# Kernel tuning notes

Hardware: AMD Instinct MI355X
Metric: run time of the kernel (lower is better)

The kernel has to match this reference:

```python
import jax, jax.numpy as jnp
import numpy as np

D_MODEL, D_STATE, D_CONV, D_INNER, DT_RANK, K = 96, 16, 3, 192, 6, 4
B, H, W = 1, 64, 64


def setup_inputs() -> dict:
    key = jax.random.key(0)
    ks = jax.random.split(key, 10)
    x = jax.random.normal(ks[0], (B, H, W, D_MODEL), jnp.float32)
    in_proj_w = jax.random.normal(ks[1], (2 * D_INNER, D_MODEL), jnp.float32) * 0.02
    conv_w = jax.random.normal(ks[2], (D_INNER, 1, D_CONV, D_CONV), jnp.float32) * 0.1
    conv_b = jnp.zeros((D_INNER,), jnp.float32)
    x_proj_w = jax.random.normal(ks[3], (K, DT_RANK + 2 * D_STATE, D_INNER), jnp.float32) * 0.02
    dt_std = DT_RANK ** -0.5
    dt_w = jax.random.uniform(ks[4], (K, D_INNER, DT_RANK), jnp.float32, -dt_std, dt_std)
    # dt bias init: inv-softplus of dt ~ logUniform(1e-3, 1e-1)
    u = jax.random.uniform(ks[5], (K, D_INNER), jnp.float32)
    dt = jnp.exp(u * (np.log(0.1) - np.log(0.001)) + np.log(0.001)).clip(1e-4)
    dt_b = dt + jnp.log(-jnp.expm1(-dt))
    A_logs = jnp.log(jnp.broadcast_to(jnp.arange(1, D_STATE + 1, dtype=jnp.float32), (K * D_INNER, D_STATE)))
    Ds = jnp.ones((K * D_INNER,), jnp.float32)
    ln_g = jnp.ones((D_INNER,), jnp.float32)
    ln_b = jnp.zeros((D_INNER,), jnp.float32)
    out_proj_w = jax.random.normal(ks[6], (D_MODEL, D_INNER), jnp.float32) * 0.02
    return dict(x=x, in_proj_w=in_proj_w, conv_w=conv_w, conv_b=conv_b, x_proj_w=x_proj_w,
                dt_w=dt_w, dt_b=dt_b, A_logs=A_logs, Ds=Ds, ln_g=ln_g, ln_b=ln_b,
                out_proj_w=out_proj_w)


def _ss2d(x, in_proj_w, conv_w, conv_b, x_proj_w, dt_w, dt_b, A_logs, Ds, ln_g, ln_b, out_proj_w):
    b, h, w, c = x.shape
    L = h * w
    d = conv_w.shape[0]            # d_inner
    n = A_logs.shape[1]            # d_state
    r = dt_w.shape[2]              # dt_rank
    # in_proj + split
    xz = jnp.einsum('bhwc,ec->bhwe', x, in_proj_w)
    xx, z = xz[..., :d], xz[..., d:]
    # depthwise conv (NCHW) + SiLU
    xc = xx.transpose(0, 3, 1, 2)
    pad = (D_CONV - 1) // 2
    xc = jax.lax.conv_general_dilated(xc, conv_w, (1, 1), [(pad, pad), (pad, pad)],
                                      feature_group_count=d) + conv_b[None, :, None, None]
    xc = jax.nn.silu(xc)
    # 4 scan directions: HW, WH, and their reverses
    x_hw = xc.reshape(b, d, L)
    x_wh = xc.transpose(0, 1, 3, 2).reshape(b, d, L)
    xs = jnp.stack([x_hw, x_wh, x_hw[..., ::-1], x_wh[..., ::-1]], axis=1)  # (b,K,d,L)
    x_dbl = jnp.einsum('bkdl,kcd->bkcl', xs, x_proj_w)
    dts, Bs, Cs = x_dbl[:, :, :r], x_dbl[:, :, r:r + n], x_dbl[:, :, r + n:]
    dts = jnp.einsum('bkrl,kdr->bkdl', dts, dt_w)
    delta = jax.nn.softplus(dts + dt_b[None, :, :, None])        # (b,K,d,L)
    A = -jnp.exp(A_logs).reshape(K, d, n)
    # time-major scanned inputs
    dA = jnp.exp(jnp.einsum('bkdl,kdn->lbkdn', delta, A))        # (L,b,K,d,n)
    dBu = jnp.einsum('bkdl,bknl,bkdl->lbkdn', delta, Bs, xs)
    Ct = Cs.transpose(3, 0, 1, 2)                                # (L,b,K,n)
    def step(hst, inp):
        dA_t, dBu_t, C_t = inp
        hst = dA_t * hst + dBu_t
        return hst, jnp.einsum('bkdn,bkn->bkd', hst, C_t)
    h0 = jnp.zeros((b, K, d, n), jnp.float32)
    _, ys = jax.lax.scan(step, h0, (dA, dBu, Ct))                # ys: (L,b,K,d)
    out_y = ys.transpose(1, 2, 3, 0) + xs * Ds.reshape(K, d)[None, :, :, None]
    # recombine directions
    inv = out_y[:, 2:4][..., ::-1]
    y1 = out_y[:, 0]
    y2 = inv[:, 0]
    wh = out_y[:, 1].reshape(b, d, w, h).transpose(0, 1, 3, 2).reshape(b, d, L)
    invwh = inv[:, 1].reshape(b, d, w, h).transpose(0, 1, 3, 2).reshape(b, d, L)
    y = (y1 + y2 + wh + invwh).transpose(0, 2, 1).reshape(b, h, w, d)
    # LayerNorm (eps=1e-5, torch default)
    mu = y.mean(-1, keepdims=True)
    var = ((y - mu) ** 2).mean(-1, keepdims=True)
    y = (y - mu) * jax.lax.rsqrt(var + 1e-5) * ln_g + ln_b
    y = y * jax.nn.silu(z)
    return jnp.einsum('bhwd,cd->bhwc', y, out_proj_w)


def reference(x, in_proj_w, conv_w, conv_b, x_proj_w, dt_w, dt_b, A_logs, Ds, ln_g, ln_b, out_proj_w):
    return _ss2d(x, in_proj_w, conv_w, conv_b, x_proj_w, dt_w, dt_b, A_logs, Ds, ln_g, ln_b, out_proj_w)
```

## Files before the change

### kernel.cpp

```cpp
#include <hip/hip_runtime.h>
#include <hip/hip_bf16.h>

#define LL 4096
#define DM 96
#define DI 192
#define NS 16
#define RK 6
#define RKP 8
#define KD 4
#define CPROJ 38
#define NCH (KD*DI)
#define NC (KD*DI*NS)
#define PT 32
#define WS 196
#define OT 8
#define CHB 7
#define CHN (1<<CHB)
#define CS (LL>>CHB)
#define L2E 1.44269504f

__device__ __forceinline__ float bf2f(unsigned short u){
  unsigned int x = ((unsigned int)u) << 16;
  return __uint_as_float(x);
}
__device__ __forceinline__ float b2f(__hip_bfloat16 v){ return __bfloat162float(v); }

__device__ __forceinline__ void detect_bf16(const unsigned short* __restrict__ xh, int tid, int* sflag){
  if (tid < 64){
    unsigned short u = xh[2*tid];
    int e = (u >> 7) & 0xFF;
    int sane = (e >= 107 && e <= 131) ? 1 : 0;
    unsigned long long m = __ballot(sane);
    if (tid == 0) *sflag = (__popcll(m) >= 32) ? 1 : 0;
  }
}

__device__ __forceinline__ int dir_map(int k, int t){
  if (k==0) return t;
  if (k==1) return ((t&63)<<6) | (t>>6);
  if (k==2) return 4095 - t;
  int u = 4095 - t; return ((u&63)<<6) | (u>>6);
}

struct P12 { const void* p[12]; };

__global__ void __launch_bounds__(384) k_inprojcvt(P12 ptrs, float* __restrict__ cvt,
                         float* __restrict__ xx, float* __restrict__ z) {
  __shared__ float xr[8*DM];
  __shared__ int sflag;
  int tid = threadIdx.x;
  detect_bf16((const unsigned short*)ptrs.p[0], tid, &sflag);
  __syncthreads();
  int f = sflag;
  if (blockIdx.x >= LL/8){
    const int off[12] = {0,36864,38592,38784,67968,72576,73344,85632,86400,86592,86784,105216};
    int i = (blockIdx.x - LL/8)*384 + tid + 36864;
    if (i < 105216){
      int j = 1;
      #pragma unroll
      for (int s = 2; s < 11; s++) if (i >= off[s]) j = s;
      int e = i - off[j];
      const void* src = ptrs.p[j+1];
      cvt[i] = f ? b2f(((const __hip_bfloat16*)src)[e]) : ((const float*)src)[e];
    }
    return;
  }
  int l0 = blockIdx.x * 8;
  if (f){
    const __hip_bfloat16* xb = (const __hip_bfloat16*)ptrs.p[0] + (size_t)l0*DM;
    for (int i = tid; i < 8*DM; i += 384) xr[i] = b2f(xb[i]);
  } else {
    const float* xf = (const float*)ptrs.p[0] + (size_t)l0*DM;
    for (int i = tid; i < 8*DM; i += 384) xr[i] = xf[i];
  }
  __syncthreads();
  int e = tid;
  float acc[8];
  #pragma unroll
  for (int i=0;i<8;i++) acc[i]=0.f;
  const float4* xr4 = (const float4*)xr;
  if (f){
    const ushort4* wb = (const ushort4*)((const unsigned short*)ptrs.p[1] + (size_t)e*DM);
    #pragma unroll 4
    for (int c4=0;c4<DM/4;c4++){
      ushort4 uv = wb[c4];
      float4 wv = make_float4(bf2f(uv.x), bf2f(uv.y), bf2f(uv.z), bf2f(uv.w));
      #pragma unroll
      for (int i=0;i<8;i++){
        float4 xv = xr4[i*24 + c4];
        acc[i] = fmaf(wv.x,xv.x,fmaf(wv.y,xv.y,fmaf(wv.z,xv.z,fmaf(wv.w,xv.w,acc[i]))));
      }
    }
  } else {
    const float4* wr4 = (const float4*)((const float*)ptrs.p[1] + (size_t)e*DM);
    #pragma unroll 4
    for (int c4=0;c4<DM/4;c4++){
      float4 wv = wr4[c4];
      #pragma unroll
      for (int i=0;i<8;i++){
        float4 xv = xr4[i*24 + c4];
        acc[i] = fmaf(wv.x,xv.x,fmaf(wv.y,xv.y,fmaf(wv.z,xv.z,fmaf(wv.w,xv.w,acc[i]))));
      }
    }
  }
  if (e < DI) {
    #pragma unroll
    for (int i=0;i<8;i++) xx[(l0+i)*DI + e] = acc[i];
  } else {
    int e2 = e - DI;
    #pragma unroll
    for (int i=0;i<8;i++) z[(l0+i)*DI + e2] = acc[i];
  }
}

__global__ void k_conv(const float* __restrict__ xx,
                       const float* __restrict__ cw,
                       const float* __restrict__ cb,
                       float* __restrict__ xc) {
  int l = blockIdx.x;
  int d = threadIdx.x;
  int h = l >> 6, w = l & 63;
  float acc = cb[d];
  #pragma unroll
  for (int ki=0; ki<3; ki++){
    int hh = h + ki - 1;
    if ((unsigned)hh >= 64u) continue;
    #pragma unroll
    for (int kj=0;kj<3;kj++){
      int wj = w + kj - 1;
      if ((unsigned)wj >= 64u) continue;
      acc = fmaf(cw[d*9 + ki*3 + kj], xx[(hh*64+wj)*DI + d], acc);
    }
  }
  xc[l*DI + d] = acc / (1.f + __expf(-acc));
}

template<int MODE>
__global__ void __launch_bounds__(256) k_projscan(
                      const float* __restrict__ xc,
                      const float* __restrict__ xpw,
                      const float* __restrict__ A_logs,
                      const float* __restrict__ dtw,
                      const float* __restrict__ dtb,
                      float* __restrict__ cumDbuf,
                      float* __restrict__ Harr,
                      float* __restrict__ ydir) {
  __shared__ float wl[CPROJ*WS];
  __shared__ float xs[PT*WS];
  __shared__ float ds_[PT*RKP];
  __shared__ float Bs[PT*NS];
  __shared__ float Cs[PT*NS];
  int b = blockIdx.x;
  int k = b >> 7;
  int c = b & 127;
  int t_base = c * PT;
  int tid = threadIdx.x;

  for (int idx = tid; idx < CPROJ*DI; idx += 256){
    int cc = idx / DI, j = idx - cc*DI;
    wl[cc*WS + j] = xpw[(k*CPROJ + cc)*DI + j];
  }
  for (int idx = tid; idx < PT*DI; idx += 256){
    int tt = idx / DI, j = idx - tt*DI;
    xs[tt*WS + j] = xc[(size_t)dir_map(k, t_base + tt)*DI + j];
  }
  __syncthreads();

  {
    int tg = tid & 7;
    int ty = tid >> 3;
    int cc0 = ty;
    int has2 = (ty + 32 < CPROJ);
    int cc1 = has2 ? (ty + 32) : ty;
    float a0x=0.f,a0y=0.f,a0z=0.f,a0w=0.f;
    float a1x=0.f,a1y=0.f,a1z=0.f,a1w=0.f;
    const float4* w0p = (const float4*)&wl[cc0*WS];
    const float4* w1p = (const float4*)&wl[cc1*WS];
    const float4* x0p = (const float4*)&xs[(tg     )*WS];
    const float4* x1p = (const float4*)&xs[(tg +  8)*WS];
    const float4* x2p = (const float4*)&xs[(tg + 16)*WS];
    const float4* x3p = (const float4*)&xs[(tg + 24)*WS];
    #pragma unroll 4
    for (int jc = 0; jc < DI/4; jc++){
      float4 w0 = w0p[jc], w1 = w1p[jc];
      float4 x0 = x0p[jc], x1 = x1p[jc], x2 = x2p[jc], x3 = x3p[jc];
      a0x = fmaf(w0.x,x0.x,fmaf(w0.y,x0.y,fmaf(w0.z,x0.z,fmaf(w0.w,x0.w,a0x))));
      a0y = fmaf(w0.x,x1.x,fmaf(w0.y,x1.y,fmaf(w0.z,x1.z,fmaf(w0.w,x1.w,a0y))));
      a0z = fmaf(w0.x,x2.x,fmaf(w0.y,x2.y,fmaf(w0.z,x2.z,fmaf(w0.w,x2.w,a0z))));
      a0w = fmaf(w0.x,x3.x,fmaf(w0.y,x3.y,fmaf(w0.z,x3.z,fmaf(w0.w,x3.w,a0w))));
      a1x = fmaf(w1.x,x0.x,fmaf(w1.y,x0.y,fmaf(w1.z,x0.z,fmaf(w1.w,x0.w,a1x))));
      a1y = fmaf(w1.x,x1.x,fmaf(w1.y,x1.y,fmaf(w1.z,x1.z,fmaf(w1.w,x1.w,a1y))));
      a1z = fmaf(w1.x,x2.x,fmaf(w1.y,x2.y,fmaf(w1.z,x2.z,fmaf(w1.w,x2.w,a1z))));
      a1w = fmaf(w1.x,x3.x,fmaf(w1.y,x3.y,fmaf(w1.z,x3.z,fmaf(w1.w,x3.w,a1w))));
    }
    float accs0[4] = {a0x,a0y,a0z,a0w};
    float accs1[4] = {a1x,a1y,a1z,a1w};
    #pragma unroll
    for (int i=0;i<4;i++){
      int t = tg + 8*i;
      {
        int cc = cc0; float v = accs0[i];
        if (cc < RK)            ds_[t*RKP + cc] = v;
        else if (cc < RK+NS)    Bs [t*NS + (cc-RK)] = v;
        else                    Cs [t*NS + (cc-RK-NS)] = v;
      }
      if (has2){
        int cc = ty + 32; float v = accs1[i];
        if (cc < RK+NS)         Bs [t*NS + (cc-RK)] = v;
        else                    Cs [t*NS + (cc-RK-NS)] = v;
      }
    }
  }
  __syncthreads();

  if (tid < DI){
    int d = tid;
    int kd = k*DI + d;
    float bt = dtb[kd];
    float w0 = dtw[kd*RK+0], w1 = dtw[kd*RK+1], w2 = dtw[kd*RK+2];
    float w3 = dtw[kd*RK+3], w4 = dtw[kd*RK+4], w5 = dtw[kd*RK+5];
    float A2[16], h[16];
    {
      const float4* ap = (const float4*)&A_logs[kd*NS];
      #pragma unroll
      for (int i=0;i<4;i++){
        float4 av = ap[i];
        A2[4*i+0] = -__expf(av.x)*L2E; A2[4*i+1] = -__expf(av.y)*L2E;
        A2[4*i+2] = -__expf(av.z)*L2E; A2[4*i+3] = -__expf(av.w)*L2E;
      }
    }
    if (MODE == 0){
      #pragma unroll
      for (int n=0;n<16;n++) h[n] = 0.f;
    } else {
      const float4* hp = (const float4*)(Harr + ((size_t)c*NCH + kd)*16);
      float4 h0 = hp[0], h1 = hp[1], h2 = hp[2], h3 = hp[3];
      h[0]=h0.x; h[1]=h0.y; h[2]=h0.z; h[3]=h0.w;
      h[4]=h1.x; h[5]=h1.y; h[6]=h1.z; h[7]=h1.w;
      h[8]=h2.x; h[9]=h2.y; h[10]=h2.z; h[11]=h2.w;
      h[12]=h3.x; h[13]=h3.y; h[14]=h3.z; h[15]=h3.w;
    }
    float cumD = 0.f;
    #pragma unroll 2
    for (int s=0; s<CS; s++){
      float4 lo = *(const float4*)(ds_ + s*RKP);
      float4 hi = *(const float4*)(ds_ + s*RKP + 4);
      float v = bt;
      v = fmaf(w0, lo.x, v); v = fmaf(w1, lo.y, v); v = fmaf(w2, lo.z, v);
      v = fmaf(w3, lo.w, v); v = fmaf(w4, hi.x, v); v = fmaf(w5, hi.y, v);
      float sp = (v > 20.f) ? v : __logf(1.f + __expf(v));
      if (MODE == 0) cumD += sp;
      float sx = sp * xs[s*WS + d];
      float4 b0 = *(const float4*)(Bs + s*NS);
      float4 b1 = *(const float4*)(Bs + s*NS + 4);
      float4 b2 = *(const float4*)(Bs + s*NS + 8);
      float4 b3 = *(const float4*)(Bs + s*NS + 12);
      float bb[16] = {b0.x,b0.y,b0.z,b0.w, b1.x,b1.y,b1.z,b1.w,
                      b2.x,b2.y,b2.z,b2.w, b3.x,b3.y,b3.z,b3.w};
      #pragma unroll
      for (int n=0;n<16;n++){
        float aa = exp2f(sp*A2[n]);
        h[n] = fmaf(aa, h[n], sx*bb[n]);
      }
      if (MODE == 1){
        float4 c0 = *(const float4*)(Cs + s*NS);
        float4 c1 = *(const float4*)(Cs + s*NS + 4);
        float4 c2 = *(const float4*)(Cs + s*NS + 8);
        float4 c3 = *(const float4*)(Cs + s*NS + 12);
        float cc[16] = {c0.x,c0.y,c0.z,c0.w, c1.x,c1.y,c1.z,c1.w,
                        c2.x,c2.y,c2.z,c2.w, c3.x,c3.y,c3.z,c3.w};
        float y0=0.f, y1=0.f, y2=0.f, y3=0.f;
        #pragma unroll
        for (int n=0;n<4;n++){
          y0 = fmaf(h[4*n+0], cc[4*n+0], y0);
          y1 = fmaf(h[4*n+1], cc[4*n+1], y1);
          y2 = fmaf(h[4*n+2], cc[4*n+2], y2);
          y3 = fmaf(h[4*n+3], cc[4*n+3], y3);
        }
        int row = dir_map(k, t_base + s);
        ydir[((size_t)k*LL + row)*DI + d] = (y0+y1)+(y2+y3);
      }
    }
    if (MODE == 0){
      cumDbuf[(size_t)c*NCH + kd] = cumD;
      float4* hp = (float4*)(Harr + ((size_t)c*NCH + kd)*16);
      hp[0] = make_float4(h[0],h[1],h[2],h[3]);
      hp[1] = make_float4(h[4],h[5],h[6],h[7]);
      hp[2] = make_float4(h[8],h[9],h[10],h[11]);
      hp[3] = make_float4(h[12],h[13],h[14],h[15]);
    }
  }
}

template<int CB>
__global__ void __launch_bounds__(512) k_scan2(const float* __restrict__ A_logs,
                                               const float* __restrict__ cumDbuf,
                                               float* __restrict__ Harr) {
  constexpr int CH = 1 << CB;
  constexpr int CHP = CH + 1;
  __shared__ float hs[64][CHP];
  __shared__ float cds[4][CH];
  int tid = threadIdx.x;
  int base = blockIdx.x * 64;
  int kd0 = blockIdx.x * 4;
  for (int i4 = tid; i4 < 16*CH; i4 += 512){
    int c = i4 >> 4;
    int jv = (i4 & 15) * 4;
    float4 v = *(const float4*)&Harr[(size_t)c*NC + base + jv];
    hs[jv][c] = v.x; hs[jv+1][c] = v.y; hs[jv+2][c] = v.z; hs[jv+3][c] = v.w;
  }
  for (int i = tid; i < 4*CH; i += 512){
    int c = i >> 2, kdl = i & 3;
    cds[kdl][c] = cumDbuf[(size_t)c*NCH + kd0 + kdl];
  }
  __syncthreads();
  if (tid < 64){
    float A2 = -__expf(A_logs[base + tid]) * L2E;
    const float* cd = cds[tid >> 4];
    float* hr = hs[tid];
    float h = 0.f;
    #pragma unroll 4
    for (int c = 0; c < CH; c++){
      float hl = hr[c];
      float P = exp2f(A2 * cd[c]);
      hr[c] = h;
      h = fmaf(P, h, hl);
    }
  }
  __syncthreads();
  for (int i4 = tid; i4 < 16*CH; i4 += 512){
    int c = i4 >> 4;
    int jv = (i4 & 15) * 4;
    float4 v = make_float4(hs[jv][c], hs[jv+1][c], hs[jv+2][c], hs[jv+3][c]);
    *(float4*)&Harr[(size_t)c*NC + base + jv] = v;
  }
}

__global__ void __launch_bounds__(192) k_out(
                      const float* __restrict__ ydir,
                      const float* __restrict__ xc,
                      const float* __restrict__ z,
                      const float* __restrict__ Ds,
                      const float* __restrict__ ln_g,
                      const float* __restrict__ ln_b,
                      const float* __restrict__ opw,
                      void* __restrict__ out,
                      const unsigned short* __restrict__ xh) {
  __shared__ float gs[OT*WS];
  __shared__ float ps[2][OT][24];
  __shared__ float mv[2][OT];
  __shared__ int sflag;
  int tid = threadIdx.x;
  int d = tid;
  detect_bf16(xh, tid, &sflag);
  int l0 = blockIdx.x * OT;
  float dsum = Ds[d] + Ds[DI+d] + Ds[2*DI+d] + Ds[3*DI+d];
  #pragma unroll
  for (int r=0;r<OT;r++){
    size_t ld = (size_t)(l0+r)*DI + d;
    float y = ydir[ld]
            + ydir[(size_t)LL*DI   + ld]
            + ydir[(size_t)2*LL*DI + ld]
            + ydir[(size_t)3*LL*DI + ld];
    gs[r*WS + d] = fmaf(xc[ld], dsum, y);
  }
  __syncthreads();
  {
    int r = tid / 24, lane = tid - r*24;
    float s1 = 0.f, s2 = 0.f;
    #pragma unroll
    for (int j = lane; j < DI; j += 24){
      float v = gs[r*WS + j];
      s1 += v; s2 += v*v;
    }
    ps[0][r][lane] = s1; ps[1][r][lane] = s2;
  }
  __syncthreads();
  if (tid < OT){
    float a = 0.f, bb = 0.f;
    #pragma unroll
    for (int j=0;j<24;j++){ a += ps[0][tid][j]; bb += ps[1][tid][j]; }
    float mu = a * (1.f/192.f);
    float var = bb * (1.f/192.f) - mu*mu;
    mv[0][tid] = mu; mv[1][tid] = rsqrtf(var + 1e-5f);
  }
  __syncthreads();
  float lg = ln_g[d], lb = ln_b[d];
  #pragma unroll
  for (int r=0;r<OT;r++){
    float yn = (gs[r*WS + d] - mv[0][r]) * mv[1][r] * lg + lb;
    float zv = z[(size_t)(l0+r)*DI + d];
    gs[r*WS + d] = yn * (zv / (1.f + __expf(-zv)));
  }
  __syncthreads();
  int half = tid / 96;
  int e = tid - half*96;
  int r0 = half*4;
  float acc[4];
  #pragma unroll
  for (int i=0;i<4;i++) acc[i] = 0.f;
  const float4* wrow = (const float4*)(opw + e*DI);
  #pragma unroll 4
  for (int jc = 0; jc < DI/4; jc++){
    float4 w = wrow[jc];
    #pragma unroll
    for (int i=0;i<4;i++){
      float4 gv = *(const float4*)&gs[(r0+i)*WS + jc*4];
      acc[i] = fmaf(w.x,gv.x,fmaf(w.y,gv.y,fmaf(w.z,gv.z,fmaf(w.w,gv.w,acc[i]))));
    }
  }
  int f = sflag;
  #pragma unroll
  for (int i=0;i<4;i++){
    int l = l0 + r0 + i;
    if (f) ((__hip_bfloat16*)out)[l*DM + e] = __float2bfloat16(acc[i]);
    else   ((float*)out)[l*DM + e] = acc[i];
  }
}

extern "C" void kernel_launch(void* const* d_in, const int* in_sizes, int n_in,
                              void* d_out, int out_size, void* d_ws, size_t ws_size,
                              hipStream_t stream) {
  float* ws = (float*)d_ws;
  float* cvt = ws + 16;
  const int off[12] = {0,36864,38592,38784,67968,72576,73344,85632,86400,86592,86784,105216};
  float* c[12];
  c[0] = nullptr;
  for (int i = 1; i < 12; i++) c[i] = cvt + off[i-1];

  float* xx   = cvt + 105216;
  float* z    = xx + (size_t)LL*DI;
  float* xc   = z  + (size_t)LL*DI;
  float* cumD = xc + (size_t)LL*DI;
  float* Harr = cumD + (size_t)CHN*NCH;
  float* ydir = Harr + (size_t)CHN*NC;

  P12 ptrs;
  for (int i = 0; i < 12; i++) ptrs.p[i] = d_in[i];

  k_inprojcvt<<<LL/8 + 178, 384, 0, stream>>>(ptrs, cvt, xx, z);
  k_conv<<<LL, DI, 0, stream>>>(xx, c[2], c[3], xc);
  k_projscan<0><<<KD*CHN, 256, 0, stream>>>(xc, c[4], c[7], c[5], c[6],
                                            cumD, Harr, nullptr);
  k_scan2<CHB><<<NCH/4, 512, 0, stream>>>(c[7], cumD, Harr);
  k_projscan<1><<<KD*CHN, 256, 0, stream>>>(xc, c[4], c[7], c[5], c[6],
                                            cumD, Harr, ydir);
  k_out<<<LL/OT, 192, 0, stream>>>(ydir, xc, z, c[8], c[9], c[10], c[11], d_out,
                                   (const unsigned short*)d_in[0]);
}
```

Measured before the change: 202.2 us.

## Split scan state across two threads per channel and skip unused C projection in pass one

The chunked scan kernel now runs 384 threads, with two threads per inner channel each owning 8 of the 16 state elements. This halves the serial per-thread work and raises parallelism. In MODE 1 the partial C-dot outputs are combined through shared memory (reusing the weight buffer) with a block barrier every 8 steps. In MODE 0 the projection skips computing C rows, which the first pass never uses. The trade-off is extra barriers and shared-memory traffic, plus duplicated softplus/dt computation in both halves.

```diff
diff --git a/kernel.cpp b/kernel.cpp
--- a/kernel.cpp
+++ b/kernel.cpp
@@ -136,7 +136,7 @@
 }
 
 template<int MODE>
-__global__ void __launch_bounds__(256) k_projscan(
+__global__ void __launch_bounds__(384, 3) k_projscan(
                       const float* __restrict__ xc,
                       const float* __restrict__ xpw,
                       const float* __restrict__ A_logs,
@@ -156,21 +156,22 @@
   int t_base = c * PT;
   int tid = threadIdx.x;
 
-  for (int idx = tid; idx < CPROJ*DI; idx += 256){
+  for (int idx = tid; idx < CPROJ*DI; idx += 384){
     int cc = idx / DI, j = idx - cc*DI;
     wl[cc*WS + j] = xpw[(k*CPROJ + cc)*DI + j];
   }
-  for (int idx = tid; idx < PT*DI; idx += 256){
+  for (int idx = tid; idx < PT*DI; idx += 384){
     int tt = idx / DI, j = idx - tt*DI;
     xs[tt*WS + j] = xc[(size_t)dir_map(k, t_base + tt)*DI + j];
   }
   __syncthreads();
 
-  {
+  if (tid < 256){
     int tg = tid & 7;
     int ty = tid >> 3;
     int cc0 = ty;
-    int has2 = (ty + 32 < CPROJ);
+    int need0 = (MODE == 0) ? (cc0 < RK+NS) : 1;
+    int has2 = (MODE == 0) ? 0 : (ty + 32 < CPROJ);
     int cc1 = has2 ? (ty + 32) : ty;
     float a0x=0.f,a0y=0.f,a0z=0.f,a0w=0.f;
     float a1x=0.f,a1y=0.f,a1z=0.f,a1w=0.f;
@@ -180,32 +181,36 @@
     const float4* x1p = (const float4*)&xs[(tg +  8)*WS];
     const float4* x2p = (const float4*)&xs[(tg + 16)*WS];
     const float4* x3p = (const float4*)&xs[(tg + 24)*WS];
-    #pragma unroll 4
-    for (int jc = 0; jc < DI/4; jc++){
-      float4 w0 = w0p[jc], w1 = w1p[jc];
-      float4 x0 = x0p[jc], x1 = x1p[jc], x2 = x2p[jc], x3 = x3p[jc];
-      a0x = fmaf(w0.x,x0.x,fmaf(w0.y,x0.y,fmaf(w0.z,x0.z,fmaf(w0.w,x0.w,a0x))));
-      a0y = fmaf(w0.x,x1.x,fmaf(w0.y,x1.y,fmaf(w0.z,x1.z,fmaf(w0.w,x1.w,a0y))));
-      a0z = fmaf(w0.x,x2.x,fmaf(w0.y,x2.y,fmaf(w0.z,x2.z,fmaf(w0.w,x2.w,a0z))));
-      a0w = fmaf(w0.x,x3.x,fmaf(w0.y,x3.y,fmaf(w0.z,x3.z,fmaf(w0.w,x3.w,a0w))));
-      a1x = fmaf(w1.x,x0.x,fmaf(w1.y,x0.y,fmaf(w1.z,x0.z,fmaf(w1.w,x0.w,a1x))));
-      a1y = fmaf(w1.x,x1.x,fmaf(w1.y,x1.y,fmaf(w1.z,x1.z,fmaf(w1.w,x1.w,a1y))));
-      a1z = fmaf(w1.x,x2.x,fmaf(w1.y,x2.y,fmaf(w1.z,x2.z,fmaf(w1.w,x2.w,a1z))));
-      a1w = fmaf(w1.x,x3.x,fmaf(w1.y,x3.y,fmaf(w1.z,x3.z,fmaf(w1.w,x3.w,a1w))));
+    if (need0){
+      #pragma unroll 4
+      for (int jc = 0; jc < DI/4; jc++){
+        float4 w0 = w0p[jc], w1 = w1p[jc];
+        float4 x0 = x0p[jc], x1 = x1p[jc], x2 = x2p[jc], x3 = x3p[jc];
+        a0x = fmaf(w0.x,x0.x,fmaf(w0.y,x0.y,fmaf(w0.z,x0.z,fmaf(w0.w,x0.w,a0x))));
+        a0y = fmaf(w0.x,x1.x,fmaf(w0.y,x1.y,fmaf(w0.z,x1.z,fmaf(w0.w,x1.w,a0y))));
+        a0z = fmaf(w0.x,x2.x,fmaf(w0.y,x2.y,fmaf(w0.z,x2.z,fmaf(w0.w,x2.w,a0z))));
+        a0w = fmaf(w0.x,x3.x,fmaf(w0.y,x3.y,fmaf(w0.z,x3.z,fmaf(w0.w,x3.w,a0w))));
+        if (has2){
+          a1x = fmaf(w1.x,x0.x,fmaf(w1.y,x0.y,fmaf(w1.z,x0.z,fmaf(w1.w,x0.w,a1x))));
+          a1y = fmaf(w1.x,x1.x,fmaf(w1.y,x1.y,fmaf(w1.z,x1.z,fmaf(w1.w,x1.w,a1y))));
+          a1z = fmaf(w1.x,x2.x,fmaf(w1.y,x2.y,fmaf(w1.z,x2.z,fmaf(w1.w,x2.w,a1z))));
+          a1w = fmaf(w1.x,x3.x,fmaf(w1.y,x3.y,fmaf(w1.z,x3.z,fmaf(w1.w,x3.w,a1w))));
+        }
+      }
     }
     float accs0[4] = {a0x,a0y,a0z,a0w};
     float accs1[4] = {a1x,a1y,a1z,a1w};
     #pragma unroll
     for (int i=0;i<4;i++){
       int t = tg + 8*i;
-      {
+      if (need0){
         int cc = cc0; float v = accs0[i];
         if (cc < RK)            ds_[t*RKP + cc] = v;
         else if (cc < RK+NS)    Bs [t*NS + (cc-RK)] = v;
         else                    Cs [t*NS + (cc-RK-NS)] = v;
       }
       if (has2){
-        int cc = ty + 32; float v = accs1[i];
+        int cc = cc1; float v = accs1[i];
         if (cc < RK+NS)         Bs [t*NS + (cc-RK)] = v;
         else                    Cs [t*NS + (cc-RK-NS)] = v;
       }
@@ -213,81 +218,88 @@
   }
   __syncthreads();
 
-  if (tid < DI){
-    int d = tid;
+  {
+    int half = (tid >= DI) ? 1 : 0;
+    int d = tid - half*DI;
     int kd = k*DI + d;
+    int n0 = half*8;
     float bt = dtb[kd];
     float w0 = dtw[kd*RK+0], w1 = dtw[kd*RK+1], w2 = dtw[kd*RK+2];
     float w3 = dtw[kd*RK+3], w4 = dtw[kd*RK+4], w5 = dtw[kd*RK+5];
-    float A2[16], h[16];
+    float A2[8], h[8];
     {
-      const float4* ap = (const float4*)&A_logs[kd*NS];
-      #pragma unroll
-      for (int i=0;i<4;i++){
-        float4 av = ap[i];
-        A2[4*i+0] = -__expf(av.x)*L2E; A2[4*i+1] = -__expf(av.y)*L2E;
-        A2[4*i+2] = -__expf(av.z)*L2E; A2[4*i+3] = -__expf(av.w)*L2E;
-      }
+      const float4* ap = (const float4*)&A_logs[kd*NS] + half*2;
+      float4 a0 = ap[0], a1 = ap[1];
+      A2[0] = -__expf(a0.x)*L2E; A2[1] = -__expf(a0.y)*L2E;
+      A2[2] = -__expf(a0.z)*L2E; A2[3] = -__expf(a0.w)*L2E;
+      A2[4] = -__expf(a1.x)*L2E; A2[5] = -__expf(a1.y)*L2E;
+      A2[6] = -__expf(a1.z)*L2E; A2[7] = -__expf(a1.w)*L2E;
     }
     if (MODE == 0){
       #pragma unroll
-      for (int n=0;n<16;n++) h[n] = 0.f;
+      for (int n=0;n<8;n++) h[n] = 0.f;
     } else {
-      const float4* hp = (const float4*)(Harr + ((size_t)c*NCH + kd)*16);
-      float4 h0 = hp[0], h1 = hp[1], h2 = hp[2], h3 = hp[3];
+      const float4* hp = (const float4*)(Harr + ((size_t)c*NCH + kd)*16) + half*2;
+      float4 h0 = hp[0], h1 = hp[1];
       h[0]=h0.x; h[1]=h0.y; h[2]=h0.z; h[3]=h0.w;
       h[4]=h1.x; h[5]=h1.y; h[6]=h1.z; h[7]=h1.w;
-      h[8]=h2.x; h[9]=h2.y; h[10]=h2.z; h[11]=h2.w;
-      h[12]=h3.x; h[13]=h3.y; h[14]=h3.z; h[15]=h3.w;
     }
     float cumD = 0.f;
-    #pragma unroll 2
-    for (int s=0; s<CS; s++){
-      float4 lo = *(const float4*)(ds_ + s*RKP);
-      float4 hi = *(const float4*)(ds_ + s*RKP + 4);
-      float v = bt;
-      v = fmaf(w0, lo.x, v); v = fmaf(w1, lo.y, v); v = fmaf(w2, lo.z, v);
-      v = fmaf(w3, lo.w, v); v = fmaf(w4, hi.x, v); v = fmaf(w5, hi.y, v);
-      float sp = (v > 20.f) ? v : __logf(1.f + __expf(v));
-      if (MODE == 0) cumD += sp;
-      float sx = sp * xs[s*WS + d];
-      float4 b0 = *(const float4*)(Bs + s*NS);
-      float4 b1 = *(const float4*)(Bs + s*NS + 4);
-      float4 b2 = *(const float4*)(Bs + s*NS + 8);
-      float4 b3 = *(const float4*)(Bs + s*NS + 12);
-      float bb[16] = {b0.x,b0.y,b0.z,b0.w, b1.x,b1.y,b1.z,b1.w,
-                      b2.x,b2.y,b2.z,b2.w, b3.x,b3.y,b3.z,b3.w};
+    float* ybuf = wl;
+    #pragma unroll
+    for (int g=0; g<4; g++){
+      float yp[8];
       #pragma unroll
-      for (int n=0;n<16;n++){
-        float aa = exp2f(sp*A2[n]);
-        h[n] = fmaf(aa, h[n], sx*bb[n]);
+      for (int si=0; si<8; si++){
+        int s = g*8 + si;
+        float4 lo = *(const float4*)(ds_ + s*RKP);
+        float4 hi = *(const float4*)(ds_ + s*RKP + 4);
+        float v = bt;
+        v = fmaf(w0, lo.x, v); v = fmaf(w1, lo.y, v); v = fmaf(w2, lo.z, v);
+        v = fmaf(w3, lo.w, v); v = fmaf(w4, hi.x, v); v = fmaf(w5, hi.y, v);
+        float sp = (v > 20.f) ? v : __logf(1.f + __expf(v));
+        if (MODE == 0) cumD += sp;
+        float sx = sp * xs[s*WS + d];
+        float4 b0 = *(const float4*)(Bs + s*NS + n0);
+        float4 b1 = *(const float4*)(Bs + s*NS + n0 + 4);
+        float bb[8] = {b0.x,b0.y,b0.z,b0.w, b1.x,b1.y,b1.z,b1.w};
+        #pragma unroll
+        for (int n=0;n<8;n++){
+          float aa = exp2f(sp*A2[n]);
+          h[n] = fmaf(aa, h[n], sx*bb[n]);
+        }
+        if (MODE == 1){
+          float4 c0 = *(const float4*)(Cs + s*NS + n0);
+          float4 c1 = *(const float4*)(Cs + s*NS + n0 + 4);
+          float cc4[8] = {c0.x,c0.y,c0.z,c0.w, c1.x,c1.y,c1.z,c1.w};
+          float y0 = fmaf(h[4], cc4[4], h[0]*cc4[0]);
+          float y1 = fmaf(h[5], cc4[5], h[1]*cc4[1]);
+          float y2 = fmaf(h[6], cc4[6], h[2]*cc4[2]);
+          float y3 = fmaf(h[7], cc4[7], h[3]*cc4[3]);
+          yp[si] = (y0+y1)+(y2+y3);
+        }
       }
       if (MODE == 1){
-        float4 c0 = *(const float4*)(Cs + s*NS);
-        float4 c1 = *(const float4*)(Cs + s*NS + 4);
-        float4 c2 = *(const float4*)(Cs + s*NS + 8);
-        float4 c3 = *(const float4*)(Cs + s*NS + 12);
-        float cc[16] = {c0.x,c0.y,c0.z,c0.w, c1.x,c1.y,c1.z,c1.w,
-                        c2.x,c2.y,c2.z,c2.w, c3.x,c3.y,c3.z,c3.w};
-        float y0=0.f, y1=0.f, y2=0.f, y3=0.f;
-        #pragma unroll
-        for (int n=0;n<4;n++){
-          y0 = fmaf(h[4*n+0], cc[4*n+0], y0);
-          y1 = fmaf(h[4*n+1], cc[4*n+1], y1);
-          y2 = fmaf(h[4*n+2], cc[4*n+2], y2);
-          y3 = fmaf(h[4*n+3], cc[4*n+3], y3);
+        if (half == 1){
+          #pragma unroll
+          for (int si=0; si<8; si++) ybuf[(g*8+si)*WS + d] = yp[si];
         }
-        int row = dir_map(k, t_base + s);
-        ydir[((size_t)k*LL + row)*DI + d] = (y0+y1)+(y2+y3);
+        __syncthreads();
+        if (half == 0){
+          #pragma unroll
+          for (int si=0; si<8; si++){
+            int s = g*8 + si;
+            int row = dir_map(k, t_base + s);
+            ydir[((size_t)k*LL + row)*DI + d] = yp[si] + ybuf[s*WS + d];
+          }
+        }
       }
     }
     if (MODE == 0){
-      cumDbuf[(size_t)c*NCH + kd] = cumD;
-      float4* hp = (float4*)(Harr + ((size_t)c*NCH + kd)*16);
+      if (half == 0) cumDbuf[(size_t)c*NCH + kd] = cumD;
+      float4* hp = (float4*)(Harr + ((size_t)c*NCH + kd)*16) + half*2;
       hp[0] = make_float4(h[0],h[1],h[2],h[3]);
       hp[1] = make_float4(h[4],h[5],h[6],h[7]);
-      hp[2] = make_float4(h[8],h[9],h[10],h[11]);
-      hp[3] = make_float4(h[12],h[13],h[14],h[15]);
     }
   }
 }
@@ -440,10 +452,10 @@
 
   k_inprojcvt<<<LL/8 + 178, 384, 0, stream>>>(ptrs, cvt, xx, z);
   k_conv<<<LL, DI, 0, stream>>>(xx, c[2], c[3], xc);
-  k_projscan<0><<<KD*CHN, 256, 0, stream>>>(xc, c[4], c[7], c[5], c[6],
+  k_projscan<0><<<KD*CHN, 384, 0, stream>>>(xc, c[4], c[7], c[5], c[6],
                                             cumD, Harr, nullptr);
   k_scan2<CHB><<<NCH/4, 512, 0, stream>>>(c[7], cumD, Harr);
-  k_projscan<1><<<KD*CHN, 256, 0, stream>>>(xc, c[4], c[7], c[5], c[6],
+  k_projscan<1><<<KD*CHN, 384, 0, stream>>>(xc, c[4], c[7], c[5], c[6],
                                             cumD, Harr, ydir);
   k_out<<<LL/OT, 192, 0, stream>>>(ydir, xc, z, c[8], c[9], c[10], c[11], d_out,
                                    (const unsigned short*)d_in[0]);
```

Result: slower. 258.8 us (+28.0%).
